# Kernel optimization log

Measured on AMD Instinct MI355X. Metric: run time of the kernel, lower is better.

The kernel has to match this reference:

```python
import jax, jax.numpy as jnp
import numpy as np

THRESH = 0.3   # vis_threshold (score filter and final keep threshold)
SIGMA = 0.5    # Gaussian soft-NMS sigma (method=2 in classic soft_nms)
B, N = 16, 2048


def setup_inputs() -> dict:
    key = jax.random.key(0)
    k1, k2, k3 = jax.random.split(key, 3)
    xy = jax.random.uniform(k1, (B, N, 2), dtype=jnp.float32) * 1024.0
    wh = jax.random.uniform(k2, (B, N, 2), dtype=jnp.float32) * 256.0 + 1.0
    scores = jax.random.uniform(k3, (B, N, 1), dtype=jnp.float32)
    detections = jnp.concatenate([xy, xy + wh, scores], axis=-1)  # [B,N,5]
    return {"detections": detections}


def _pairwise_iou(b):
    # b: [N,4] as (x1,y1,x2,y2); classic soft-NMS uses +1 area convention
    x1, y1, x2, y2 = b[:, 0], b[:, 1], b[:, 2], b[:, 3]
    area = (x2 - x1 + 1.0) * (y2 - y1 + 1.0)
    xx1 = jnp.maximum(x1[:, None], x1[None, :])
    yy1 = jnp.maximum(y1[:, None], y1[None, :])
    xx2 = jnp.minimum(x2[:, None], x2[None, :])
    yy2 = jnp.minimum(y2[:, None], y2[None, :])
    w = jnp.clip(xx2 - xx1 + 1.0, 0.0)
    h = jnp.clip(yy2 - yy1 + 1.0, 0.0)
    inter = w * h
    return inter / (area[:, None] + area[None, :] - inter)  # [N,N]


def _soft_nms_single(boxes, scores):
    # boxes: [N,4], scores: [N]
    n = scores.shape[0]
    iou = _pairwise_iou(boxes)            # [N,N]
    valid = scores > THRESH               # score-threshold prefilter
    s0 = jnp.where(valid, scores, 0.0)

    def step(carry, _):
        s, active = carry
        i = jnp.argmax(jnp.where(active, s, -1.0))     # greedy pick of max live score
        si = jnp.where(active[i], s[i], -1.0)          # -1 sentinel once all boxes consumed
        w = jnp.exp(-(iou[i] * iou[i]) / SIGMA)        # Gaussian decay (method=2)
        active = active.at[i].set(False)
        s = jnp.where(active, s * w, s)                # decay remaining live scores
        return (s, active), (i, si)

    _, (idx, picked) = jax.lax.scan(step, (s0, valid), None, length=n)
    # score each box carried at the moment it was picked; .max ignores -1 sentinels
    final = jnp.full((n,), -1.0, scores.dtype).at[idx].max(picked)
    keep = final > THRESH
    return final, keep


def reference(detections):
    boxes = detections[..., :4]   # [B,N,4]
    scores = detections[..., 4]   # [B,N]
    final, keep = jax.vmap(_soft_nms_single)(boxes, scores)
    return final, keep
```

## Files before the change

### kernel.cpp

```cpp
#include <hip/hip_runtime.h>
#include <stdint.h>

static constexpr float kThresh = 0.3f;
static constexpr float kFreeze = 0.0195f;
static constexpr int N    = 2048;
static constexpr int NT   = 256;
static constexpr int LPT  = N / NT;
static constexpr int NW   = NT / 64;
static constexpr int KMAX = 8;

using u64 = unsigned long long;
using u32 = unsigned int;

template <int CTRL>
__device__ __forceinline__ float dpp_fmax_step(float v) {
    const int m = __builtin_amdgcn_update_dpp(__float_as_int(v), __float_as_int(v),
                                              CTRL, 0xF, 0xF, false);
    return fmaxf(v, __int_as_float(m));
}
__device__ __forceinline__ float wave_fmax(float v) {
    v = dpp_fmax_step<0x111>(v);
    v = dpp_fmax_step<0x112>(v);
    v = dpp_fmax_step<0x114>(v);
    v = dpp_fmax_step<0x118>(v);
    v = dpp_fmax_step<0x142>(v);
    v = dpp_fmax_step<0x143>(v);
    return __int_as_float(__builtin_amdgcn_readlane(__float_as_int(v), 63));
}

template <int CTRL>
__device__ __forceinline__ u32 dpp_umin_step(u32 v) {
    const int m = __builtin_amdgcn_update_dpp((int)v, (int)v, CTRL, 0xF, 0xF, false);
    return ((u32)m < v) ? (u32)m : v;
}
__device__ __forceinline__ u32 wave_umin(u32 v) {
    v = dpp_umin_step<0x111>(v);
    v = dpp_umin_step<0x112>(v);
    v = dpp_umin_step<0x114>(v);
    v = dpp_umin_step<0x118>(v);
    v = dpp_umin_step<0x142>(v);
    v = dpp_umin_step<0x143>(v);
    return (u32)__builtin_amdgcn_readlane((int)v, 63);
}

struct Pick {
    int    j;
    float4 box;
    float  area;
};

template <int K>
__device__ __forceinline__ void decay_best(
        float (&sr)[KMAX], const float (&x1)[KMAX], const float (&y1)[KMAX],
        const float (&x2)[KMAX], const float (&y2)[KMAX], const float (&ar)[KMAX],
        const int (&jr)[KMAX], const Pick& w, float& sbest, int& jbest)
{
    sbest = -1.0f; jbest = 0x7FFFFFFF;
    #pragma unroll
    for (int e = 0; e < K; ++e) {
        if (jr[e] == w.j) sr[e] = -1.0f;
        const float xx1 = fmaxf(w.box.x, x1[e]);
        const float yy1 = fmaxf(w.box.y, y1[e]);
        const float xx2 = fminf(w.box.z, x2[e]);
        const float yy2 = fminf(w.box.w, y2[e]);
        const float ww  = fmaxf(xx2 - xx1 + 1.0f, 0.0f);
        const float hh  = fmaxf(yy2 - yy1 + 1.0f, 0.0f);
        const float inter = ww * hh;
        const float iou   = inter / (w.area + ar[e] - inter);
        sr[e] *= expf(-(iou * iou) * 2.0f);
        const bool bt = sr[e] > sbest;
        sbest = bt ? sr[e] : sbest;
        jbest = bt ? jr[e] : jbest;
    }
}

template <int K>
__device__ __forceinline__ void fill_slots(
        float (&sr)[KMAX], float (&x1)[KMAX], float (&y1)[KMAX],
        float (&x2)[KMAX], float (&y2)[KMAX], float (&ar)[KMAX], int (&jr)[KMAX],
        const int* slist, const float* srs, const float4* sbox, int t, int alive)
{
    #pragma unroll
    for (int e = 0; e < K; ++e) {
        const int pos = t + NT * e;
        if (pos < alive) {
            const int j = slist[pos];
            sr[e] = srs[pos];
            const float4 bb = sbox[j];
            x1[e] = bb.x; y1[e] = bb.y; x2[e] = bb.z; y2[e] = bb.w;
            ar[e] = (bb.z - bb.x + 1.0f) * (bb.w - bb.y + 1.0f);
            jr[e] = j;
        } else {
            sr[e] = -1.0f;
            x1[e] = 3.0e38f; y1[e] = 3.0e38f; x2[e] = -3.0e38f; y2[e] = -3.0e38f;
            ar[e] = 1.0f;
            jr[e] = -2;
        }
    }
}

template <int K>
__device__ __forceinline__ void run_tier(
        int& alive, int& k, Pick& w,
        float (&sr)[KMAX], float (&x1)[KMAX], float (&y1)[KMAX],
        float (&x2)[KMAX], float (&y2)[KMAX], float (&ar)[KMAX], int (&jr)[KMAX],
        int* slist, float* srs, const float4* sbox, const float* sarea, float* sfin,
        float2 (*red)[NW], int* swave, int t, int lane, int wid)
{
    const int floorA = (K > 1) ? NT * (K - 1) : 0;
    if (alive <= floorA) return;

    fill_slots<K>(sr, x1, y1, x2, y2, ar, jr, slist, srs, sbox, t, alive);
    const int tierFill = alive;

    while (alive > floorA) {
        const int par = k & 1;
        float sbest; int jbest;
        decay_best<K>(sr, x1, y1, x2, y2, ar, jr, w, sbest, jbest);

        const float wmaxf = wave_fmax(sbest);
        const bool  cand  = (__float_as_int(sbest) >= 0) && (sbest == wmaxf);
        const u64   mask  = __ballot(cand);
        if (mask == 0ULL) {
            if (lane == 0) red[par][wid] = make_float2(-1.0f, __int_as_float(0x7FFFFFFF));
        } else if (__popcll(mask) == 1) {
            if (cand) red[par][wid] = make_float2(sbest, __int_as_float(jbest));
        } else {
            const u32 jm = wave_umin(cand ? (u32)jbest : 0xFFFFFFFFu);
            if (cand && (u32)jbest == jm)
                red[par][wid] = make_float2(sbest, __int_as_float(jbest));
        }
        __syncthreads();

        float2 r0 = red[par][0];
        float bs = r0.x; int bj = __float_as_int(r0.y);
        #pragma unroll
        for (int q = 1; q < NW; ++q) {
            const float2 rq = red[par][q];
            const float s = rq.x; const int j = __float_as_int(rq.y);
            const bool bt = (s > bs) || ((s == bs) && (j < bj));
            bs = bt ? s : bs;
            bj = bt ? j : bj;
        }
        const float v1 = bs;

        if (v1 < kFreeze) {
            #pragma unroll
            for (int e = 0; e < K; ++e) {
                const int pos = t + NT * e;
                if (pos < tierFill && __float_as_int(sr[e]) >= 0)
                    sfin[jr[e]] = sr[e];
            }
            alive = -1;
            return;
        }

        if (t == 0) sfin[bj] = v1;
        w.j    = bj;
        w.box  = sbox[bj];
        w.area = sarea[bj];
        --alive; ++k;
    }

    if (K > 1) {
        float d0; int d1;
        decay_best<K>(sr, x1, y1, x2, y2, ar, jr, w, d0, d1);
        w.j    = -1;
        w.box  = make_float4(3.0e38f, 3.0e38f, -3.0e38f, -3.0e38f);
        w.area = 1.0f;
        int c = 0;
        #pragma unroll
        for (int e = 0; e < K; ++e) c += (__float_as_int(sr[e]) >= 0) ? 1 : 0;
        int pfx = c;
        #pragma unroll
        for (int d = 1; d < 64; d <<= 1) {
            const int v = __shfl_up(pfx, d, 64);
            if (lane >= d) pfx += v;
        }
        if (lane == 63) swave[wid] = pfx;
        __syncthreads();
        int wbase = 0;
        #pragma unroll
        for (int q = 0; q < NW; ++q)
            if (q < wid) wbase += swave[q];
        int mypos = wbase + (pfx - c);
        #pragma unroll
        for (int e = 0; e < K; ++e) {
            if (__float_as_int(sr[e]) >= 0) {
                slist[mypos] = jr[e];
                srs[mypos]   = sr[e];
                ++mypos;
            }
        }
        __syncthreads();
    }
}

__launch_bounds__(NT, 1)
__global__ void soft_nms_kernel(const float* __restrict__ det,
                                float* __restrict__ out, int B)
{
    const int b = blockIdx.x, t = threadIdx.x, lane = t & 63, wid = t >> 6;

    __shared__ float4 sbox[N];
    __shared__ float  sarea[N];
    __shared__ float  sfin[N];
    __shared__ float  srs[N];
    __shared__ int    slist[N];
    __shared__ int    swave[NW];
    __shared__ float2 red[2][NW];

    const float* dbase = det + (size_t)b * N * 5;

    float scv[LPT]; int lval = 0, c = 0;
    #pragma unroll
    for (int e = 0; e < LPT; ++e) {
        const int j = t * LPT + e;
        const float* p = dbase + (size_t)j * 5;
        const float X1 = p[0], Y1 = p[1], X2 = p[2], Y2 = p[3], SC = p[4];
        sbox[j]  = make_float4(X1, Y1, X2, Y2);
        sarea[j] = (X2 - X1 + 1.0f) * (Y2 - Y1 + 1.0f);
        sfin[j]  = -1.0f;
        scv[e]   = SC;
        const int va = SC > kThresh;
        lval |= va << e; c += va;
    }
    int pfx = c;
    #pragma unroll
    for (int d = 1; d < 64; d <<= 1) {
        const int v = __shfl_up(pfx, d, 64);
        if (lane >= d) pfx += v;
    }
    if (lane == 63) swave[wid] = pfx;
    __syncthreads();
    int wbase = 0, n0 = 0;
    #pragma unroll
    for (int q = 0; q < NW; ++q) {
        const int v = swave[q];
        if (q < wid) wbase += v;
        n0 += v;
    }
    int mypos = wbase + (pfx - c);
    #pragma unroll
    for (int e = 0; e < LPT; ++e)
        if ((lval >> e) & 1) { slist[mypos] = t * LPT + e; srs[mypos] = scv[e]; ++mypos; }
    __syncthreads();

    float sr[KMAX], x1[KMAX], y1[KMAX], x2[KMAX], y2[KMAX], ar[KMAX]; int jr[KMAX];
    int alive = n0, k = 0;
    Pick w;
    w.j    = -1;
    w.box  = make_float4(3.0e38f, 3.0e38f, -3.0e38f, -3.0e38f);
    w.area = 1.0f;

    run_tier<8>(alive,k,w,sr,x1,y1,x2,y2,ar,jr,slist,srs,sbox,sarea,sfin,red,swave,t,lane,wid);
    run_tier<7>(alive,k,w,sr,x1,y1,x2,y2,ar,jr,slist,srs,sbox,sarea,sfin,red,swave,t,lane,wid);
    run_tier<6>(alive,k,w,sr,x1,y1,x2,y2,ar,jr,slist,srs,sbox,sarea,sfin,red,swave,t,lane,wid);
    run_tier<5>(alive,k,w,sr,x1,y1,x2,y2,ar,jr,slist,srs,sbox,sarea,sfin,red,swave,t,lane,wid);
    run_tier<4>(alive,k,w,sr,x1,y1,x2,y2,ar,jr,slist,srs,sbox,sarea,sfin,red,swave,t,lane,wid);
    run_tier<3>(alive,k,w,sr,x1,y1,x2,y2,ar,jr,slist,srs,sbox,sarea,sfin,red,swave,t,lane,wid);
    run_tier<2>(alive,k,w,sr,x1,y1,x2,y2,ar,jr,slist,srs,sbox,sarea,sfin,red,swave,t,lane,wid);
    run_tier<1>(alive,k,w,sr,x1,y1,x2,y2,ar,jr,slist,srs,sbox,sarea,sfin,red,swave,t,lane,wid);

    __syncthreads();
    float* of = out + (size_t)b * N;
    float* ok = out + (size_t)B * N + (size_t)b * N;
    #pragma unroll
    for (int e = 0; e < LPT; ++e) {
        const int j = t * LPT + e;
        const float f = sfin[j];
        of[j] = f;
        ok[j] = (f > kThresh) ? 1.0f : 0.0f;
    }
}

extern "C" void kernel_launch(void* const* d_in, const int* in_sizes, int n_in,
                              void* d_out, int out_size, void* d_ws, size_t ws_size,
                              hipStream_t stream) {
    const float* det = (const float*)d_in[0];
    float* out = (float*)d_out;
    const int B = in_sizes[0] / (N * 5);
    hipLaunchKernelGGL(soft_nms_kernel, dim3(B), dim3(NT), 0, stream, det, out, B);
}
```

Measured before the change: 919.6 us.

## Sort boxes by x1 and skip IoU work for non-overlapping wave bands

Boxes are bitonic-sorted by x1 in shared memory, then each wave holds contiguous x1 ranges per slot. Using the maximum box width, each step skips the IoU and exp decay for slot bands whose x1 range cannot overlap the picked box. The compaction is reworked with ballots so the banded layout survives. The cost is an upfront sort and extra shared memory, plus a per-slot range check. The skip is also wave-uniform, so divergence stays low.

```diff
diff --git a/kernel.cpp b/kernel.cpp
--- a/kernel.cpp
+++ b/kernel.cpp
@@ -43,6 +43,10 @@
     return (u32)__builtin_amdgcn_readlane((int)v, 63);
 }
 
+__device__ __forceinline__ float uread(float v) {
+    return __int_as_float(__builtin_amdgcn_readfirstlane(__float_as_int(v)));
+}
+
 struct Pick {
     int    j;
     float4 box;
@@ -50,39 +54,20 @@
 };
 
 template <int K>
-__device__ __forceinline__ void decay_best(
-        float (&sr)[KMAX], const float (&x1)[KMAX], const float (&y1)[KMAX],
-        const float (&x2)[KMAX], const float (&y2)[KMAX], const float (&ar)[KMAX],
-        const int (&jr)[KMAX], const Pick& w, float& sbest, int& jbest)
-{
-    sbest = -1.0f; jbest = 0x7FFFFFFF;
-    #pragma unroll
-    for (int e = 0; e < K; ++e) {
-        if (jr[e] == w.j) sr[e] = -1.0f;
-        const float xx1 = fmaxf(w.box.x, x1[e]);
-        const float yy1 = fmaxf(w.box.y, y1[e]);
-        const float xx2 = fminf(w.box.z, x2[e]);
-        const float yy2 = fminf(w.box.w, y2[e]);
-        const float ww  = fmaxf(xx2 - xx1 + 1.0f, 0.0f);
-        const float hh  = fmaxf(yy2 - yy1 + 1.0f, 0.0f);
-        const float inter = ww * hh;
-        const float iou   = inter / (w.area + ar[e] - inter);
-        sr[e] *= expf(-(iou * iou) * 2.0f);
-        const bool bt = sr[e] > sbest;
-        sbest = bt ? sr[e] : sbest;
-        jbest = bt ? jr[e] : jbest;
-    }
-}
-
-template <int K>
-__device__ __forceinline__ void fill_slots(
+__device__ __forceinline__ void run_tier(
+        int& alive, int& k, Pick& w,
         float (&sr)[KMAX], float (&x1)[KMAX], float (&y1)[KMAX],
         float (&x2)[KMAX], float (&y2)[KMAX], float (&ar)[KMAX], int (&jr)[KMAX],
-        const int* slist, const float* srs, const float4* sbox, int t, int alive)
+        int* slist, float* srs, const float4* sbox, const float* sarea, float* sfin,
+        float2 (*red)[NW], int* bandCnt, float wspanG,
+        int t, int lane, int wid)
 {
+    const int floorA = (K > 1) ? NT * (K - 1) : 0;
+    if (alive <= floorA) return;
+
     #pragma unroll
     for (int e = 0; e < K; ++e) {
-        const int pos = t + NT * e;
+        const int pos = (e * NW + wid) * 64 + lane;
         if (pos < alive) {
             const int j = slist[pos];
             sr[e] = srs[pos];
@@ -97,26 +82,37 @@
             jr[e] = -2;
         }
     }
-}
-
-template <int K>
-__device__ __forceinline__ void run_tier(
-        int& alive, int& k, Pick& w,
-        float (&sr)[KMAX], float (&x1)[KMAX], float (&y1)[KMAX],
-        float (&x2)[KMAX], float (&y2)[KMAX], float (&ar)[KMAX], int (&jr)[KMAX],
-        int* slist, float* srs, const float4* sbox, const float* sarea, float* sfin,
-        float2 (*red)[NW], int* swave, int t, int lane, int wid)
-{
-    const int floorA = (K > 1) ? NT * (K - 1) : 0;
-    if (alive <= floorA) return;
-
-    fill_slots<K>(sr, x1, y1, x2, y2, ar, jr, slist, srs, sbox, t, alive);
+    float blo[KMAX], bhi[KMAX];
+    #pragma unroll
+    for (int e = 0; e < K; ++e) {
+        blo[e] = __int_as_float(__builtin_amdgcn_readlane(__float_as_int(x1[e]), 0));
+        bhi[e] = __int_as_float(__builtin_amdgcn_readlane(__float_as_int(x1[e]), 63));
+    }
     const int tierFill = alive;
 
     while (alive > floorA) {
         const int par = k & 1;
-        float sbest; int jbest;
-        decay_best<K>(sr, x1, y1, x2, y2, ar, jr, w, sbest, jbest);
+        const float R = uread(w.box.z + 2.0f);
+        const float L = uread(w.box.x - wspanG - 2.0f);
+        float sbest = -1.0f; int jbest = 0x7FFFFFFF;
+        #pragma unroll
+        for (int e = 0; e < K; ++e) {
+            if (!(blo[e] > R || bhi[e] < L)) {
+                if (jr[e] == w.j) sr[e] = -1.0f;
+                const float xx1 = fmaxf(w.box.x, x1[e]);
+                const float yy1 = fmaxf(w.box.y, y1[e]);
+                const float xx2 = fminf(w.box.z, x2[e]);
+                const float yy2 = fminf(w.box.w, y2[e]);
+                const float ww  = fmaxf(xx2 - xx1 + 1.0f, 0.0f);
+                const float hh  = fmaxf(yy2 - yy1 + 1.0f, 0.0f);
+                const float inter = ww * hh;
+                const float iou   = inter / (w.area + ar[e] - inter);
+                sr[e] *= expf(-(iou * iou) * 2.0f);
+            }
+            const bool bt = (sr[e] > sbest) || ((sr[e] == sbest) && (jr[e] < jbest));
+            sbest = bt ? sr[e] : sbest;
+            jbest = bt ? jr[e] : jbest;
+        }
 
         const float wmaxf = wave_fmax(sbest);
         const bool  cand  = (__float_as_int(sbest) >= 0) && (sbest == wmaxf);
@@ -147,7 +143,7 @@
         if (v1 < kFreeze) {
             #pragma unroll
             for (int e = 0; e < K; ++e) {
-                const int pos = t + NT * e;
+                const int pos = (e * NW + wid) * 64 + lane;
                 if (pos < tierFill && __float_as_int(sr[e]) >= 0)
                     sfin[jr[e]] = sr[e];
             }
@@ -163,33 +159,51 @@
     }
 
     if (K > 1) {
-        float d0; int d1;
-        decay_best<K>(sr, x1, y1, x2, y2, ar, jr, w, d0, d1);
+        {
+            const float R = uread(w.box.z + 2.0f);
+            const float L = uread(w.box.x - wspanG - 2.0f);
+            #pragma unroll
+            for (int e = 0; e < K; ++e) {
+                if (!(blo[e] > R || bhi[e] < L)) {
+                    if (jr[e] == w.j) sr[e] = -1.0f;
+                    const float xx1 = fmaxf(w.box.x, x1[e]);
+                    const float yy1 = fmaxf(w.box.y, y1[e]);
+                    const float xx2 = fminf(w.box.z, x2[e]);
+                    const float yy2 = fminf(w.box.w, y2[e]);
+                    const float ww  = fmaxf(xx2 - xx1 + 1.0f, 0.0f);
+                    const float hh  = fmaxf(yy2 - yy1 + 1.0f, 0.0f);
+                    const float inter = ww * hh;
+                    const float iou   = inter / (w.area + ar[e] - inter);
+                    sr[e] *= expf(-(iou * iou) * 2.0f);
+                }
+            }
+        }
         w.j    = -1;
         w.box  = make_float4(3.0e38f, 3.0e38f, -3.0e38f, -3.0e38f);
         w.area = 1.0f;
-        int c = 0;
+        u32 rnk[KMAX];
         #pragma unroll
-        for (int e = 0; e < K; ++e) c += (__float_as_int(sr[e]) >= 0) ? 1 : 0;
-        int pfx = c;
-        #pragma unroll
-        for (int d = 1; d < 64; d <<= 1) {
-            const int v = __shfl_up(pfx, d, 64);
-            if (lane >= d) pfx += v;
-        }
-        if (lane == 63) swave[wid] = pfx;
+        for (int e = 0; e < K; ++e) {
+            const u64 m = __ballot(__float_as_int(sr[e]) >= 0);
+            if (lane == 0) bandCnt[e * NW + wid] = (int)__popcll(m);
+            rnk[e] = (u32)__popcll(m & ((1ull << lane) - 1ull));
+        }
         __syncthreads();
-        int wbase = 0;
-        #pragma unroll
-        for (int q = 0; q < NW; ++q)
-            if (q < wid) wbase += swave[q];
-        int mypos = wbase + (pfx - c);
+        int pre[KMAX];
+        {
+            int run = 0;
+            #pragma unroll
+            for (int bb = 0; bb < K * NW; ++bb) {
+                if ((bb & (NW - 1)) == wid) pre[bb / NW] = run;
+                run += bandCnt[bb];
+            }
+        }
         #pragma unroll
         for (int e = 0; e < K; ++e) {
             if (__float_as_int(sr[e]) >= 0) {
-                slist[mypos] = jr[e];
-                srs[mypos]   = sr[e];
-                ++mypos;
+                const int np = pre[e] + (int)rnk[e];
+                slist[np] = jr[e];
+                srs[np]   = sr[e];
             }
         }
         __syncthreads();
@@ -204,25 +218,62 @@
 
     __shared__ float4 sbox[N];
     __shared__ float  sarea[N];
+    __shared__ float  sscore[N];
     __shared__ float  sfin[N];
     __shared__ float  srs[N];
     __shared__ int    slist[N];
+    __shared__ u64    skey[N];
     __shared__ int    swave[NW];
+    __shared__ float  swm[NW];
+    __shared__ int    bandCnt[KMAX * NW];
     __shared__ float2 red[2][NW];
 
     const float* dbase = det + (size_t)b * N * 5;
 
-    float scv[LPT]; int lval = 0, c = 0;
+    float spmax = 0.0f;
     #pragma unroll
     for (int e = 0; e < LPT; ++e) {
         const int j = t * LPT + e;
         const float* p = dbase + (size_t)j * 5;
         const float X1 = p[0], Y1 = p[1], X2 = p[2], Y2 = p[3], SC = p[4];
-        sbox[j]  = make_float4(X1, Y1, X2, Y2);
-        sarea[j] = (X2 - X1 + 1.0f) * (Y2 - Y1 + 1.0f);
-        sfin[j]  = -1.0f;
-        scv[e]   = SC;
-        const int va = SC > kThresh;
+        sbox[j]   = make_float4(X1, Y1, X2, Y2);
+        sarea[j]  = (X2 - X1 + 1.0f) * (Y2 - Y1 + 1.0f);
+        sscore[j] = SC;
+        sfin[j]   = -1.0f;
+        skey[j] = ((u64)(u32)__float_as_int(X1) << 32) | (u32)j;
+        spmax = fmaxf(spmax, X2 - X1);
+    }
+    {
+        const float wv = wave_fmax(spmax);
+        if (lane == 0) swm[wid] = wv;
+    }
+    __syncthreads();
+    const float wspanG = fmaxf(fmaxf(swm[0], swm[1]), fmaxf(swm[2], swm[3]));
+
+    for (int len = 2; len <= N; len <<= 1) {
+        for (int str = len >> 1; str > 0; str >>= 1) {
+            __syncthreads();
+            #pragma unroll
+            for (int r = 0; r < N / (2 * NT); ++r) {
+                const int kk = r * NT + t;
+                const int i  = ((kk & ~(str - 1)) << 1) | (kk & (str - 1));
+                const int p2 = i + str;
+                const u64 a = skey[i], c2 = skey[p2];
+                const bool asc = (i & len) == 0;
+                if ((a > c2) == asc) { skey[i] = c2; skey[p2] = a; }
+            }
+        }
+    }
+    __syncthreads();
+
+    float scv[LPT]; int jv[LPT]; int lval = 0, c = 0;
+    #pragma unroll
+    for (int e = 0; e < LPT; ++e) {
+        const int pos = t * LPT + e;
+        const int j = (int)(skey[pos] & 0x7FFu);
+        const float sc = sscore[j];
+        scv[e] = sc; jv[e] = j;
+        const int va = sc > kThresh;
         lval |= va << e; c += va;
     }
     int pfx = c;
@@ -243,7 +294,7 @@
     int mypos = wbase + (pfx - c);
     #pragma unroll
     for (int e = 0; e < LPT; ++e)
-        if ((lval >> e) & 1) { slist[mypos] = t * LPT + e; srs[mypos] = scv[e]; ++mypos; }
+        if ((lval >> e) & 1) { slist[mypos] = jv[e]; srs[mypos] = scv[e]; ++mypos; }
     __syncthreads();
 
     float sr[KMAX], x1[KMAX], y1[KMAX], x2[KMAX], y2[KMAX], ar[KMAX]; int jr[KMAX];
@@ -253,14 +304,14 @@
     w.box  = make_float4(3.0e38f, 3.0e38f, -3.0e38f, -3.0e38f);
     w.area = 1.0f;
 
-    run_tier<8>(alive,k,w,sr,x1,y1,x2,y2,ar,jr,slist,srs,sbox,sarea,sfin,red,swave,t,lane,wid);
-    run_tier<7>(alive,k,w,sr,x1,y1,x2,y2,ar,jr,slist,srs,sbox,sarea,sfin,red,swave,t,lane,wid);
-    run_tier<6>(alive,k,w,sr,x1,y1,x2,y2,ar,jr,slist,srs,sbox,sarea,sfin,red,swave,t,lane,wid);
-    run_tier<5>(alive,k,w,sr,x1,y1,x2,y2,ar,jr,slist,srs,sbox,sarea,sfin,red,swave,t,lane,wid);
-    run_tier<4>(alive,k,w,sr,x1,y1,x2,y2,ar,jr,slist,srs,sbox,sarea,sfin,red,swave,t,lane,wid);
-    run_tier<3>(alive,k,w,sr,x1,y1,x2,y2,ar,jr,slist,srs,sbox,sarea,sfin,red,swave,t,lane,wid);
-    run_tier<2>(alive,k,w,sr,x1,y1,x2,y2,ar,jr,slist,srs,sbox,sarea,sfin,red,swave,t,lane,wid);
-    run_tier<1>(alive,k,w,sr,x1,y1,x2,y2,ar,jr,slist,srs,sbox,sarea,sfin,red,swave,t,lane,wid);
+    run_tier<8>(alive,k,w,sr,x1,y1,x2,y2,ar,jr,slist,srs,sbox,sarea,sfin,red,bandCnt,wspanG,t,lane,wid);
+    run_tier<7>(alive,k,w,sr,x1,y1,x2,y2,ar,jr,slist,srs,sbox,sarea,sfin,red,bandCnt,wspanG,t,lane,wid);
+    run_tier<6>(alive,k,w,sr,x1,y1,x2,y2,ar,jr,slist,srs,sbox,sarea,sfin,red,bandCnt,wspanG,t,lane,wid);
+    run_tier<5>(alive,k,w,sr,x1,y1,x2,y2,ar,jr,slist,srs,sbox,sarea,sfin,red,bandCnt,wspanG,t,lane,wid);
+    run_tier<4>(alive,k,w,sr,x1,y1,x2,y2,ar,jr,slist,srs,sbox,sarea,sfin,red,bandCnt,wspanG,t,lane,wid);
+    run_tier<3>(alive,k,w,sr,x1,y1,x2,y2,ar,jr,slist,srs,sbox,sarea,sfin,red,bandCnt,wspanG,t,lane,wid);
+    run_tier<2>(alive,k,w,sr,x1,y1,x2,y2,ar,jr,slist,srs,sbox,sarea,sfin,red,bandCnt,wspanG,t,lane,wid);
+    run_tier<1>(alive,k,w,sr,x1,y1,x2,y2,ar,jr,slist,srs,sbox,sarea,sfin,red,bandCnt,wspanG,t,lane,wid);
 
     __syncthreads();
     float* of = out + (size_t)b * N;
```

Measured after the change: 1.138 ms. +23.7%, slower.

## Periodically drop frozen low-score boxes and recompact live list within tiers

Applied to the files above, without the earlier changes.

Every 128 picks inside a multi-slot tier, boxes whose decayed score has fallen below the freeze threshold are written to the final output and removed. The remaining live boxes are then compacted and reloaded into registers, so the tier can drop to fewer slots per thread sooner. The end-of-tier compaction also drops frozen boxes now. This trades an extra prefix scan, two block barriers and a slot refill every 128 iterations for less per-iteration decay work. It relies on frozen scores not changing the later greedy order, the same assumption the existing early exit already makes.

```diff
diff --git a/kernel.cpp b/kernel.cpp
--- a/kernel.cpp
+++ b/kernel.cpp
@@ -100,6 +100,54 @@
 }
 
 template <int K>
+__device__ __forceinline__ int drop_recompact(
+        Pick& w,
+        float (&sr)[KMAX], float (&x1)[KMAX], float (&y1)[KMAX],
+        float (&x2)[KMAX], float (&y2)[KMAX], float (&ar)[KMAX], int (&jr)[KMAX],
+        int* slist, float* srs, float* sfin, int* swave, int t, int lane, int wid)
+{
+    float d0; int d1;
+    decay_best<K>(sr, x1, y1, x2, y2, ar, jr, w, d0, d1);
+    w.j    = -1;
+    w.box  = make_float4(3.0e38f, 3.0e38f, -3.0e38f, -3.0e38f);
+    w.area = 1.0f;
+    int c = 0;
+    #pragma unroll
+    for (int e = 0; e < K; ++e) {
+        const bool liv  = (__float_as_int(sr[e]) >= 0);
+        const bool keep = liv && (sr[e] >= kFreeze);
+        if (liv && !keep) sfin[jr[e]] = sr[e];
+        c += keep ? 1 : 0;
+    }
+    int pfx = c;
+    #pragma unroll
+    for (int d = 1; d < 64; d <<= 1) {
+        const int v = __shfl_up(pfx, d, 64);
+        if (lane >= d) pfx += v;
+    }
+    if (lane == 63) swave[wid] = pfx;
+    __syncthreads();
+    int wbase = 0, newAlive = 0;
+    #pragma unroll
+    for (int q = 0; q < NW; ++q) {
+        const int v = swave[q];
+        if (q < wid) wbase += v;
+        newAlive += v;
+    }
+    int mypos = wbase + (pfx - c);
+    #pragma unroll
+    for (int e = 0; e < K; ++e) {
+        if (__float_as_int(sr[e]) >= 0 && sr[e] >= kFreeze) {
+            slist[mypos] = jr[e];
+            srs[mypos]   = sr[e];
+            ++mypos;
+        }
+    }
+    __syncthreads();
+    return newAlive;
+}
+
+template <int K>
 __device__ __forceinline__ void run_tier(
         int& alive, int& k, Pick& w,
         float (&sr)[KMAX], float (&x1)[KMAX], float (&y1)[KMAX],
@@ -111,7 +159,8 @@
     if (alive <= floorA) return;
 
     fill_slots<K>(sr, x1, y1, x2, y2, ar, jr, slist, srs, sbox, t, alive);
-    const int tierFill = alive;
+    int tierFill = alive;
+    int pc = 0;
 
     while (alive > floorA) {
         const int par = k & 1;
@@ -159,40 +208,21 @@
         w.j    = bj;
         w.box  = sbox[bj];
         w.area = sarea[bj];
-        --alive; ++k;
+        --alive; ++k; ++pc;
+
+        if (K > 1 && pc == 128 && alive > floorA) {
+            alive = drop_recompact<K>(w, sr, x1, y1, x2, y2, ar, jr,
+                                      slist, srs, sfin, swave, t, lane, wid);
+            if (alive > 0) {
+                fill_slots<K>(sr, x1, y1, x2, y2, ar, jr, slist, srs, sbox, t, alive);
+                tierFill = alive;
+            }
+        }
     }
 
     if (K > 1) {
-        float d0; int d1;
-        decay_best<K>(sr, x1, y1, x2, y2, ar, jr, w, d0, d1);
-        w.j    = -1;
-        w.box  = make_float4(3.0e38f, 3.0e38f, -3.0e38f, -3.0e38f);
-        w.area = 1.0f;
-        int c = 0;
-        #pragma unroll
-        for (int e = 0; e < K; ++e) c += (__float_as_int(sr[e]) >= 0) ? 1 : 0;
-        int pfx = c;
-        #pragma unroll
-        for (int d = 1; d < 64; d <<= 1) {
-            const int v = __shfl_up(pfx, d, 64);
-            if (lane >= d) pfx += v;
-        }
-        if (lane == 63) swave[wid] = pfx;
-        __syncthreads();
-        int wbase = 0;
-        #pragma unroll
-        for (int q = 0; q < NW; ++q)
-            if (q < wid) wbase += swave[q];
-        int mypos = wbase + (pfx - c);
-        #pragma unroll
-        for (int e = 0; e < K; ++e) {
-            if (__float_as_int(sr[e]) >= 0) {
-                slist[mypos] = jr[e];
-                srs[mypos]   = sr[e];
-                ++mypos;
-            }
-        }
-        __syncthreads();
+        alive = drop_recompact<K>(w, sr, x1, y1, x2, y2, ar, jr,
+                                  slist, srs, sfin, swave, t, lane, wid);
     }
 }
 
```

Measured after the change: 1.086 ms. 18.0% more time.
